# Kernel tuning notes

Hardware: AMD Instinct MI355X
Metric: run time of the kernel (lower is better)

Reference implementation:

```python
import jax, jax.numpy as jnp
import numpy as np

QMAX = 127.0  # 8-bit symmetric: levels in [-128, 127]


def _ste_round(v):
    # round with straight-through estimator (matches torch fake-quant training)
    return v + jax.lax.stop_gradient(jnp.round(v) - v)


def _act_fake_quant(x, clip_factor):
    # per-tensor symmetric fake quant with learnable clip (lac):
    # clip range = sigmoid(clip_factor) * max|x|
    scale = jax.nn.sigmoid(clip_factor) * jnp.max(jnp.abs(x)) / QMAX
    return jnp.clip(_ste_round(x / scale), -QMAX - 1.0, QMAX) * scale


def _weight_fake_quant(w):
    # per-output-channel symmetric fake quant; w: [out, in]
    scale = jnp.max(jnp.abs(w), axis=1, keepdims=True) / QMAX
    return jnp.clip(_ste_round(w / scale), -QMAX - 1.0, QMAX) * scale


def setup_inputs() -> dict:
    key = jax.random.key(0)
    k1, k2, k3, k4 = jax.random.split(key, 4)
    B, S, H, I = 8, 8192, 1024, 2816
    return {
        "x": jax.random.normal(k1, (B, S, H), dtype=jnp.float32),
        "clip_x": jnp.full((1,), 4.0, dtype=jnp.float32),     # sigmoid(4) ~ 0.982
        "clip_down": jnp.full((1,), 4.0, dtype=jnp.float32),
        "w_gate": jax.random.normal(k2, (I, H), dtype=jnp.float32) * 0.02,
        "w_up": jax.random.normal(k3, (I, H), dtype=jnp.float32) * 0.02,
        "w_down": jax.random.normal(k4, (H, I), dtype=jnp.float32) * 0.02,
    }


def reference(x, clip_x, clip_down, w_gate, w_up, w_down):
    # _trans_forward: quantize act -> gate/up quant-matmul -> SwiGLU -> quantize -> down quant-matmul
    xq = _act_fake_quant(x, clip_x[0])                       # [B,S,H]
    gate = jnp.einsum("bsh,ih->bsi", xq, _weight_fake_quant(w_gate))
    up = jnp.einsum("bsh,ih->bsi", xq, _weight_fake_quant(w_up))
    h = _act_fake_quant(jax.nn.silu(gate) * up, clip_down[0])  # [B,S,I]
    return jnp.einsum("bsi,hi->bsh", h, _weight_fake_quant(w_down))
```

## Files before the change

kernel.cpp:

```cpp
#include <hip/hip_runtime.h>
#include <stdint.h>

typedef __attribute__((ext_vector_type(4))) int i32x4;

typedef const __attribute__((address_space(1))) void gvoid_t;
typedef __attribute__((address_space(3))) void lvoid_t;

#define GLD16(g, l) __builtin_amdgcn_global_load_lds((gvoid_t*)(g), (lvoid_t*)(l), 16, 0, 0)
#define FENCE() asm volatile("" ::: "memory")
#define BARRIER() do { FENCE(); __builtin_amdgcn_s_barrier(); FENCE(); } while (0)
#define GATE4() asm volatile("s_waitcnt vmcnt(4)\n\ts_barrier" ::: "memory")
#define GATE0() asm volatile("s_waitcnt vmcnt(0)\n\ts_barrier" ::: "memory")

__device__ inline int q1mul(float x, float r) {
    return (int)fminf(fmaxf(rintf(x * r), -128.f), 127.f);
}
__device__ inline int q1div(float x, float s) {
    return (int)fminf(fmaxf(rintf(x / s), -128.f), 127.f);
}
__device__ inline int pack4(float4 v, float r) {
    return (q1mul(v.x, r) & 255) | ((q1mul(v.y, r) & 255) << 8) |
           ((q1mul(v.z, r) & 255) << 16) | ((q1mul(v.w, r) & 255) << 24);
}

__global__ void k_absmax(const float* __restrict__ x, size_t n4, unsigned int* __restrict__ out) {
    size_t S = (size_t)gridDim.x * blockDim.x;
    size_t i = (size_t)blockIdx.x * blockDim.x + threadIdx.x;
    const float4* x4 = (const float4*)x;
    float m0 = 0.f, m1 = 0.f, m2 = 0.f, m3 = 0.f;
    for (; i + 3 * S < n4; i += 4 * S) {
        float4 v0 = x4[i], v1 = x4[i + S], v2 = x4[i + 2 * S], v3 = x4[i + 3 * S];
        m0 = fmaxf(m0, fmaxf(fmaxf(fabsf(v0.x), fabsf(v0.y)), fmaxf(fabsf(v0.z), fabsf(v0.w))));
        m1 = fmaxf(m1, fmaxf(fmaxf(fabsf(v1.x), fabsf(v1.y)), fmaxf(fabsf(v1.z), fabsf(v1.w))));
        m2 = fmaxf(m2, fmaxf(fmaxf(fabsf(v2.x), fabsf(v2.y)), fmaxf(fabsf(v2.z), fabsf(v2.w))));
        m3 = fmaxf(m3, fmaxf(fmaxf(fabsf(v3.x), fabsf(v3.y)), fmaxf(fabsf(v3.z), fabsf(v3.w))));
    }
    for (; i < n4; i += S) {
        float4 v = x4[i];
        m0 = fmaxf(m0, fmaxf(fmaxf(fabsf(v.x), fabsf(v.y)), fmaxf(fabsf(v.z), fabsf(v.w))));
    }
    float m = fmaxf(fmaxf(m0, m1), fmaxf(m2, m3));
    #pragma unroll
    for (int off = 32; off > 0; off >>= 1) m = fmaxf(m, __shfl_xor(m, off, 64));
    if ((threadIdx.x & 63) == 0) atomicMax(out, __float_as_uint(m));
}

__global__ void k_scale(const float* __restrict__ clip, const unsigned int* __restrict__ maxbits,
                        float* __restrict__ s_out) {
    float m = __uint_as_float(*maxbits);
    float sig = 1.f / (1.f + expf(-clip[0]));
    float s = sig * m / 127.f;
    s_out[0] = s;
    s_out[1] = 1.f / s;
}

__global__ void k_quant_f32_i8(const float* __restrict__ in, int4* __restrict__ out,
                               const float* __restrict__ sptr, size_t n16) {
    float r = sptr[1];
    size_t S = (size_t)gridDim.x * blockDim.x;
    size_t i = (size_t)blockIdx.x * blockDim.x + threadIdx.x;
    const float4* in4 = (const float4*)in;
    for (; i < n16; i += S) {
        float4 v0 = in4[4 * i], v1 = in4[4 * i + 1], v2 = in4[4 * i + 2], v3 = in4[4 * i + 3];
        int4 o;
        o.x = pack4(v0, r); o.y = pack4(v1, r); o.z = pack4(v2, r); o.w = pack4(v3, r);
        out[i] = o;
    }
}

__global__ void k_quant_h16_i8(const short* __restrict__ h16, const float* __restrict__ sblk,
                               const float* __restrict__ sh, int4* __restrict__ qh, size_t nchunks) {
    const float rh = sh[1] * (1.f / 32766.f);
    size_t S = (size_t)gridDim.x * blockDim.x;
    size_t i = (size_t)blockIdx.x * blockDim.x + threadIdx.x;
    for (; i < nchunks; i += S) {
        int row = (int)(i / 176);
        int col = (int)(i - (size_t)row * 176) * 16;
        float f = sblk[(row >> 8) * 22 + (col >> 7)] * rh;
        const int4* p = (const int4*)(h16 + (size_t)row * 2816 + col);
        int4 lo = p[0], hi = p[1];
        int w[8] = {lo.x, lo.y, lo.z, lo.w, hi.x, hi.y, hi.z, hi.w};
        int ob[4];
        #pragma unroll
        for (int j = 0; j < 4; ++j) {
            int q0 = q1mul((float)(short)(w[2 * j] & 0xFFFF), f);
            int q1 = q1mul((float)(short)(w[2 * j] >> 16), f);
            int q2 = q1mul((float)(short)(w[2 * j + 1] & 0xFFFF), f);
            int q3 = q1mul((float)(short)(w[2 * j + 1] >> 16), f);
            ob[j] = (q0 & 255) | ((q1 & 255) << 8) | ((q2 & 255) << 16) | ((q3 & 255) << 24);
        }
        int4 o; o.x = ob[0]; o.y = ob[1]; o.z = ob[2]; o.w = ob[3];
        qh[i] = o;
    }
}

__global__ void k_quant_w_i8(const float* __restrict__ W, int8_t* __restrict__ Q,
                             float* __restrict__ srow, int cols) {
    int row = blockIdx.x;
    const float* w = W + (size_t)row * cols;
    float m = 0.f;
    for (int c = threadIdx.x; c < cols; c += 256) m = fmaxf(m, fabsf(w[c]));
    #pragma unroll
    for (int off = 32; off > 0; off >>= 1) m = fmaxf(m, __shfl_xor(m, off, 64));
    __shared__ float red[4];
    if ((threadIdx.x & 63) == 0) red[threadIdx.x >> 6] = m;
    __syncthreads();
    if (threadIdx.x == 0) {
        float mm = fmaxf(fmaxf(red[0], red[1]), fmaxf(red[2], red[3]));
        red[0] = mm / 127.f;
        srow[row] = mm / 127.f;
    }
    __syncthreads();
    float s = red[0];
    for (int c = threadIdx.x; c < cols; c += 256)
        Q[(size_t)row * cols + c] = (int8_t)q1div(w[c], s);
}

__global__ __launch_bounds__(512, 2) void k_gemm1_i8(
    const int8_t* __restrict__ Aq, const int8_t* __restrict__ Bg, const int8_t* __restrict__ Bu,
    const float* __restrict__ sg, const float* __restrict__ su, const float* __restrict__ sx,
    short* __restrict__ H16, float* __restrict__ sblk, unsigned int* __restrict__ maxh,
    int nt_base)
{
    constexpr int K = 1024, N = 2816, NT = K / 64, TB = 32768;
    __shared__ int8_t lds[131072];

    const int wgl = (int)blockIdx.x >> 3;
    const int xcd = (int)blockIdx.x & 7;
    const int mtspan = (int)(gridDim.x >> 3) / 11;
    const int mt = xcd * mtspan + wgl / 11;
    const int nt = nt_base + wgl % 11;
    const int m0 = mt * 256, n0 = nt * 128;
    const int tid = threadIdx.x;
    const int wid = tid >> 6, lane = tid & 63;
    const int wm = wid >> 2, wn = wid & 3;
    const int lr = lane & 15, lk = lane >> 4;

    const int srow = tid >> 2;
    const int scol = ((tid & 3) ^ ((srow >> 1) & 3)) << 4;
    const int8_t* gA0 = Aq + (size_t)(m0 + srow) * K + scol;
    const int8_t* gA1 = gA0 + (size_t)128 * K;
    const int8_t* gG  = Bg + (size_t)(n0 + srow) * K + scol;
    const int8_t* gU  = Bu + (size_t)(n0 + srow) * K + scol;
    const int ldst = wid << 10;

    const int swz = (lk ^ ((lr >> 1) & 3)) << 4;
    int offA[8], offG[2], offU[2];
    #pragma unroll
    for (int mi = 0; mi < 8; ++mi) offA[mi] = (wm * 128 + mi * 16 + lr) * 64 + swz;
    #pragma unroll
    for (int ni = 0; ni < 2; ++ni) {
        offG[ni] = 16384 + (wn * 32 + ni * 16 + lr) * 64 + swz;
        offU[ni] = 24576 + (wn * 32 + ni * 16 + lr) * 64 + swz;
    }

    i32x4 accg[8][2] = {};
    i32x4 accu[8][2] = {};

    auto stage1 = [&](int t, int q) {
        int8_t* L = &lds[(t % 3) * TB];
        const size_t k0 = (size_t)t * 64;
        if (q == 0)      GLD16(gA0 + k0, L + ldst);
        else if (q == 1) GLD16(gA1 + k0, L + 8192  + ldst);
        else if (q == 2) GLD16(gG  + k0, L + 16384 + ldst);
        else             GLD16(gU  + k0, L + 24576 + ldst);
    };

    #pragma unroll
    for (int q = 0; q < 4; ++q) stage1(0, q);
    #pragma unroll
    for (int q = 0; q < 4; ++q) stage1(1, q);
    GATE4();

    for (int t = 0; t < NT; ++t) {
        const int8_t* L = &lds[(t % 3) * TB];
        const bool st2 = (t + 2 < NT);
        i32x4 bg[2], bu[2];
        #pragma unroll
        for (int q = 0; q < 4; ++q) {
            i32x4 a0 = *(const i32x4*)(L + offA[2 * q]);
            i32x4 a1 = *(const i32x4*)(L + offA[2 * q + 1]);
            if (q == 0) {
                #pragma unroll
                for (int ni = 0; ni < 2; ++ni) {
                    bg[ni] = *(const i32x4*)(L + offG[ni]);
                    bu[ni] = *(const i32x4*)(L + offU[ni]);
                }
            }
            if (st2) stage1(t + 2, q);
            BARRIER();
            __builtin_amdgcn_s_setprio(1);
            #pragma unroll
            for (int ni = 0; ni < 2; ++ni) {
                accg[2 * q][ni]     = __builtin_amdgcn_mfma_i32_16x16x64_i8(a0, bg[ni], accg[2 * q][ni], 0, 0, 0);
                accu[2 * q][ni]     = __builtin_amdgcn_mfma_i32_16x16x64_i8(a0, bu[ni], accu[2 * q][ni], 0, 0, 0);
                accg[2 * q + 1][ni] = __builtin_amdgcn_mfma_i32_16x16x64_i8(a1, bg[ni], accg[2 * q + 1][ni], 0, 0, 0);
                accu[2 * q + 1][ni] = __builtin_amdgcn_mfma_i32_16x16x64_i8(a1, bu[ni], accu[2 * q + 1][ni], 0, 0, 0);
            }
            __builtin_amdgcn_s_setprio(0);
            if (q == 3) { if (st2) { GATE4(); } else { GATE0(); } }
            else        { BARRIER(); }
        }
    }

    const float s_x = sx[0];
    float lmax = 0.f;
    #pragma unroll
    for (int ni = 0; ni < 2; ++ni) {
        const int nl = wn * 32 + ni * 16 + lr;
        const float fg = s_x * sg[n0 + nl];
        const float fu = s_x * su[n0 + nl];
        #pragma unroll
        for (int mi = 0; mi < 8; ++mi) {
            const int rowb = wm * 128 + mi * 16 + lk * 4;
            #pragma unroll
            for (int r = 0; r < 4; ++r) {
                float g = (float)accg[mi][ni][r] * fg;
                float u = (float)accu[mi][ni][r] * fu;
                float h = g * u / (1.f + expf(-g));
                *(float*)(lds + ((rowb + r) << 9) + (nl << 2)) = h;
                lmax = fmaxf(lmax, fabsf(h));
            }
        }
    }
    #pragma unroll
    for (int off = 32; off > 0; off >>= 1) lmax = fmaxf(lmax, __shfl_xor(lmax, off, 64));
    unsigned int* slot = (unsigned int*)&sblk[mt * 22 + nt];
    if (lane == 0) atomicMax(slot, __float_as_uint(lmax));
    BARRIER();
    const float bmax = __uint_as_float(*slot);
    if (tid == 0) atomicMax(maxh, __float_as_uint(bmax));
    const float qs = 32766.f / fmaxf(bmax, 1e-20f);
    uint* H16u = (uint*)H16;
    #pragma unroll
    for (int k = 0; k < 32; ++k) {
        const int fidx = 2 * (tid + k * 512);
        const int row = fidx >> 7, c2 = fidx & 127;
        const float2 hv = *(const float2*)(lds + (fidx << 2));
        const int s0 = (int)rintf(hv.x * qs), s1 = (int)rintf(hv.y * qs);
        H16u[((size_t)(m0 + row) * N + n0 + c2) >> 1] = (s0 & 0xFFFF) | (s1 << 16);
    }
}

__global__ __launch_bounds__(512, 2) void k_gemm2_i8(
    const int8_t* __restrict__ Aq, const int8_t* __restrict__ Bw,
    const float* __restrict__ sw, const float* __restrict__ sh,
    float* __restrict__ Out)
{
    constexpr int K = 2816, N = 1024, NT = K / 64, TB = 32768;
    __shared__ int8_t lds[3 * TB];

    const int chunk = gridDim.x >> 3;
    const int wg = ((int)blockIdx.x & 7) * chunk + ((int)blockIdx.x >> 3);
    const int mt = wg >> 2, nt = wg & 3;
    const int m0 = mt * 256, n0 = nt * 256;
    const int tid = threadIdx.x;
    const int wid = tid >> 6, lane = tid & 63;
    const int wm = wid >> 2, wn = wid & 3;
    const int lr = lane & 15, lk = lane >> 4;

    const int srow = tid >> 2;
    const int scol = ((tid & 3) ^ ((srow >> 1) & 3)) << 4;
    const int8_t* gA0 = Aq + (size_t)(m0 + srow) * K + scol;
    const int8_t* gA1 = gA0 + (size_t)128 * K;
    const int8_t* gB0 = Bw + (size_t)(n0 + srow) * K + scol;
    const int8_t* gB1 = gB0 + (size_t)128 * K;
    const int ldst = wid << 10;

    const int swz = (lk ^ ((lr >> 1) & 3)) << 4;
    int offA[8], offB[4];
    #pragma unroll
    for (int mi = 0; mi < 8; ++mi) offA[mi] = (wm * 128 + mi * 16 + lr) * 64 + swz;
    #pragma unroll
    for (int ni = 0; ni < 4; ++ni) offB[ni] = 16384 + (wn * 64 + ni * 16 + lr) * 64 + swz;

    i32x4 acc[8][4] = {};

    auto stage1 = [&](int t, int q) {
        int8_t* L = &lds[(t % 3) * TB];
        const size_t k0 = (size_t)t * 64;
        if (q == 0)      GLD16(gA0 + k0, L + ldst);
        else if (q == 1) GLD16(gA1 + k0, L + 8192  + ldst);
        else if (q == 2) GLD16(gB0 + k0, L + 16384 + ldst);
        else             GLD16(gB1 + k0, L + 24576 + ldst);
    };

    #pragma unroll
    for (int q = 0; q < 4; ++q) stage1(0, q);
    #pragma unroll
    for (int q = 0; q < 4; ++q) stage1(1, q);
    GATE4();

    for (int t = 0; t < NT; ++t) {
        const int8_t* L = &lds[(t % 3) * TB];
        const bool st2 = (t + 2 < NT);
        i32x4 b[4];
        #pragma unroll
        for (int q = 0; q < 4; ++q) {
            i32x4 a0 = *(const i32x4*)(L + offA[2 * q]);
            i32x4 a1 = *(const i32x4*)(L + offA[2 * q + 1]);
            if (q == 0) {
                #pragma unroll
                for (int ni = 0; ni < 4; ++ni) b[ni] = *(const i32x4*)(L + offB[ni]);
            }
            if (st2) stage1(t + 2, q);
            BARRIER();
            __builtin_amdgcn_s_setprio(1);
            #pragma unroll
            for (int ni = 0; ni < 4; ++ni) {
                acc[2 * q][ni]     = __builtin_amdgcn_mfma_i32_16x16x64_i8(a0, b[ni], acc[2 * q][ni], 0, 0, 0);
                acc[2 * q + 1][ni] = __builtin_amdgcn_mfma_i32_16x16x64_i8(a1, b[ni], acc[2 * q + 1][ni], 0, 0, 0);
            }
            __builtin_amdgcn_s_setprio(0);
            if (q == 3) { if (st2) { GATE4(); } else { GATE0(); } }
            else        { BARRIER(); }
        }
    }

    const float s_h = sh[0];
    #pragma unroll
    for (int ni = 0; ni < 4; ++ni) {
        const int n = n0 + wn * 64 + ni * 16 + lr;
        const float f = s_h * sw[n];
        #pragma unroll
        for (int mi = 0; mi < 8; ++mi) {
            const int mb = m0 + wm * 128 + mi * 16 + lk * 4;
            #pragma unroll
            for (int r = 0; r < 4; ++r)
                Out[(size_t)(mb + r) * N + n] = (float)acc[mi][ni][r] * f;
        }
    }
}

extern "C" void kernel_launch(void* const* d_in, const int* in_sizes, int n_in,
                              void* d_out, int out_size, void* d_ws, size_t ws_size,
                              hipStream_t stream) {
    const float* x       = (const float*)d_in[0];
    const float* clip_x  = (const float*)d_in[1];
    const float* clip_dn = (const float*)d_in[2];
    const float* w_gate  = (const float*)d_in[3];
    const float* w_up    = (const float*)d_in[4];
    const float* w_down  = (const float*)d_in[5];
    float* out = (float*)d_out;

    const int Hd = 1024, Id = 2816;
    const int M = in_sizes[0] / Hd;
    const size_t nx = (size_t)M * Hd;
    const size_t nh = (size_t)M * Id;

    char* ws = (char*)d_ws;
    size_t off = 0;
    auto alloc = [&](size_t bytes) -> char* {
        char* p = ws + off;
        off = (off + bytes + 255) & ~(size_t)255;
        return p;
    };
    unsigned int* max_slots = (unsigned int*)alloc(8);
    float* sxp = (float*)alloc(8);
    float* shp = (float*)alloc(8);
    int8_t* qx  = (int8_t*)alloc(nx);
    int8_t* qwg = (int8_t*)alloc((size_t)Id * Hd);
    int8_t* qwu = (int8_t*)alloc((size_t)Id * Hd);
    int8_t* qwd = (int8_t*)alloc((size_t)Hd * Id);
    float* swg = (float*)alloc((size_t)Id * 4);
    float* swu = (float*)alloc((size_t)Id * 4);
    float* swd = (float*)alloc((size_t)Hd * 4);
    int8_t* qh = (int8_t*)alloc(nh);
    short* h16 = (short*)alloc(nh * 2);
    const size_t sblk_bytes = (size_t)(M / 256) * 22 * 4;
    float* sblk = (float*)alloc(sblk_bytes);

    hipMemsetAsync(max_slots, 0, 8, stream);
    hipMemsetAsync(sblk, 0, sblk_bytes, stream);

    k_absmax<<<4096, 256, 0, stream>>>(x, nx / 4, &max_slots[0]);
    k_scale<<<1, 1, 0, stream>>>(clip_x, &max_slots[0], sxp);
    k_quant_f32_i8<<<2048, 256, 0, stream>>>(x, (int4*)qx, sxp, nx / 16);
    k_quant_w_i8<<<Id, 256, 0, stream>>>(w_gate, qwg, swg, Hd);
    k_quant_w_i8<<<Id, 256, 0, stream>>>(w_up, qwu, swu, Hd);
    k_quant_w_i8<<<Hd, 256, 0, stream>>>(w_down, qwd, swd, Id);

    const int g1grid = (M / 256) * 11;
    k_gemm1_i8<<<g1grid, 512, 0, stream>>>(qx, qwg, qwu, swg, swu, sxp, h16, sblk, &max_slots[1], 0);
    k_gemm1_i8<<<g1grid, 512, 0, stream>>>(qx, qwg, qwu, swg, swu, sxp, h16, sblk, &max_slots[1], 11);
    k_scale<<<1, 1, 0, stream>>>(clip_dn, &max_slots[1], shp);
    k_quant_h16_i8<<<4096, 256, 0, stream>>>(h16, sblk, shp, (int4*)qh, nh / 16);

    k_gemm2_i8<<<(M / 256) * (Hd / 256), 512, 0, stream>>>(qh, qwd, swd, shp, out);
}
```

Measured before the change: 1.151 ms.

## Deepen int8 GEMM pipeline to four LDS stages with inline-asm LDS reads

Both int8 GEMM kernels move from a 3-buffer to a 4-buffer LDS ring and prefetch three k-tiles ahead, with the vmcnt gates retuned to match. LDS fragment reads are now issued through inline ds_read_b128 with immediate offsets from one base address instead of per-fragment offset arrays, followed by explicit lgkmcnt waits and sched barriers. The aim is to hide more global-load latency and cut address arithmetic in the inner loop. The cost is 128KB of LDS per block, which may lower occupancy below the declared two blocks per CU. Hand-placed waits also restrict how the compiler can schedule instructions.

```diff
diff --git a/kernel.cpp b/kernel.cpp
--- a/kernel.cpp
+++ b/kernel.cpp
@@ -9,8 +9,16 @@
 #define GLD16(g, l) __builtin_amdgcn_global_load_lds((gvoid_t*)(g), (lvoid_t*)(l), 16, 0, 0)
 #define FENCE() asm volatile("" ::: "memory")
 #define BARRIER() do { FENCE(); __builtin_amdgcn_s_barrier(); FENCE(); } while (0)
+#define SBAR() asm volatile("s_barrier" ::: "memory")
+#define LGKM0() do { asm volatile("s_waitcnt lgkmcnt(0)" ::: "memory"); __builtin_amdgcn_sched_barrier(0); } while (0)
+#define GATE8() asm volatile("s_waitcnt vmcnt(8)\n\ts_barrier" ::: "memory")
 #define GATE4() asm volatile("s_waitcnt vmcnt(4)\n\ts_barrier" ::: "memory")
 #define GATE0() asm volatile("s_waitcnt vmcnt(0)\n\ts_barrier" ::: "memory")
+
+#define DSR2(d0, d1, addr, O0, O1)                                  \
+    asm volatile("ds_read_b128 %0, %2 offset:" O0 "\n\t"            \
+                 "ds_read_b128 %1, %2 offset:" O1                   \
+                 : "=v"(d0), "=v"(d1) : "v"(addr))
 
 __device__ inline int q1mul(float x, float r) {
     return (int)fminf(fmaxf(rintf(x * r), -128.f), 127.f);
@@ -145,20 +153,16 @@
     const int ldst = wid << 10;
 
     const int swz = (lk ^ ((lr >> 1) & 3)) << 4;
-    int offA[8], offG[2], offU[2];
-    #pragma unroll
-    for (int mi = 0; mi < 8; ++mi) offA[mi] = (wm * 128 + mi * 16 + lr) * 64 + swz;
-    #pragma unroll
-    for (int ni = 0; ni < 2; ++ni) {
-        offG[ni] = 16384 + (wn * 32 + ni * 16 + lr) * 64 + swz;
-        offU[ni] = 24576 + (wn * 32 + ni * 16 + lr) * 64 + swz;
-    }
+    const unsigned ldsBase = (unsigned)(size_t)&lds[0];
+    const unsigned aoff = (unsigned)((wm * 128 + lr) * 64 + swz);
+    const unsigned boff = (unsigned)(16384 + (wn * 32 + lr) * 64 + swz);
 
     i32x4 accg[8][2] = {};
     i32x4 accu[8][2] = {};
+    i32x4 bg[2], bu[2];
 
     auto stage1 = [&](int t, int q) {
-        int8_t* L = &lds[(t % 3) * TB];
+        int8_t* L = &lds[(t & 3) * TB];
         const size_t k0 = (size_t)t * 64;
         if (q == 0)      GLD16(gA0 + k0, L + ldst);
         else if (q == 1) GLD16(gA1 + k0, L + 8192  + ldst);
@@ -170,38 +174,57 @@
     for (int q = 0; q < 4; ++q) stage1(0, q);
     #pragma unroll
     for (int q = 0; q < 4; ++q) stage1(1, q);
-    GATE4();
+    #pragma unroll
+    for (int q = 0; q < 4; ++q) stage1(2, q);
+    GATE8();
+
+#define G1_MFMA(Q, A0, A1)                                                                     \
+    __builtin_amdgcn_s_setprio(1);                                                             \
+    _Pragma("unroll")                                                                          \
+    for (int ni = 0; ni < 2; ++ni) {                                                           \
+        accg[2 * (Q)][ni]     = __builtin_amdgcn_mfma_i32_16x16x64_i8(A0, bg[ni], accg[2 * (Q)][ni], 0, 0, 0);     \
+        accu[2 * (Q)][ni]     = __builtin_amdgcn_mfma_i32_16x16x64_i8(A0, bu[ni], accu[2 * (Q)][ni], 0, 0, 0);     \
+        accg[2 * (Q) + 1][ni] = __builtin_amdgcn_mfma_i32_16x16x64_i8(A1, bg[ni], accg[2 * (Q) + 1][ni], 0, 0, 0); \
+        accu[2 * (Q) + 1][ni] = __builtin_amdgcn_mfma_i32_16x16x64_i8(A1, bu[ni], accu[2 * (Q) + 1][ni], 0, 0, 0); \
+    }                                                                                          \
+    __builtin_amdgcn_s_setprio(0);
 
     for (int t = 0; t < NT; ++t) {
-        const int8_t* L = &lds[(t % 3) * TB];
-        const bool st2 = (t + 2 < NT);
-        i32x4 bg[2], bu[2];
-        #pragma unroll
-        for (int q = 0; q < 4; ++q) {
-            i32x4 a0 = *(const i32x4*)(L + offA[2 * q]);
-            i32x4 a1 = *(const i32x4*)(L + offA[2 * q + 1]);
-            if (q == 0) {
-                #pragma unroll
-                for (int ni = 0; ni < 2; ++ni) {
-                    bg[ni] = *(const i32x4*)(L + offG[ni]);
-                    bu[ni] = *(const i32x4*)(L + offU[ni]);
-                }
-            }
-            if (st2) stage1(t + 2, q);
-            BARRIER();
-            __builtin_amdgcn_s_setprio(1);
-            #pragma unroll
-            for (int ni = 0; ni < 2; ++ni) {
-                accg[2 * q][ni]     = __builtin_amdgcn_mfma_i32_16x16x64_i8(a0, bg[ni], accg[2 * q][ni], 0, 0, 0);
-                accu[2 * q][ni]     = __builtin_amdgcn_mfma_i32_16x16x64_i8(a0, bu[ni], accu[2 * q][ni], 0, 0, 0);
-                accg[2 * q + 1][ni] = __builtin_amdgcn_mfma_i32_16x16x64_i8(a1, bg[ni], accg[2 * q + 1][ni], 0, 0, 0);
-                accu[2 * q + 1][ni] = __builtin_amdgcn_mfma_i32_16x16x64_i8(a1, bu[ni], accu[2 * q + 1][ni], 0, 0, 0);
-            }
-            __builtin_amdgcn_s_setprio(0);
-            if (q == 3) { if (st2) { GATE4(); } else { GATE0(); } }
-            else        { BARRIER(); }
-        }
-    }
+        const unsigned bufb = ldsBase + ((unsigned)(t & 3) << 15);
+        const unsigned aAddr = bufb + aoff, bAddr = bufb + boff;
+        const bool st3 = (t + 3 < NT);
+        i32x4 a0, a1;
+
+        DSR2(a0, a1, aAddr, "0", "1024");
+        DSR2(bg[0], bg[1], bAddr, "0", "1024");
+        DSR2(bu[0], bu[1], bAddr, "8192", "9216");
+        if (st3) stage1(t + 3, 0);
+        SBAR(); LGKM0();
+        G1_MFMA(0, a0, a1)
+        SBAR();
+
+        DSR2(a0, a1, aAddr, "2048", "3072");
+        if (st3) stage1(t + 3, 1);
+        SBAR(); LGKM0();
+        G1_MFMA(1, a0, a1)
+        SBAR();
+
+        DSR2(a0, a1, aAddr, "4096", "5120");
+        if (st3) stage1(t + 3, 2);
+        SBAR(); LGKM0();
+        G1_MFMA(2, a0, a1)
+        SBAR();
+
+        DSR2(a0, a1, aAddr, "6144", "7168");
+        if (st3) stage1(t + 3, 3);
+        SBAR(); LGKM0();
+        G1_MFMA(3, a0, a1)
+        if (t + 3 < NT)      { GATE8(); }
+        else if (t + 2 < NT) { GATE4(); }
+        else if (t + 1 < NT) { GATE0(); }
+        else                 { SBAR(); }
+    }
+#undef G1_MFMA
 
     const float s_x = sx[0];
     float lmax = 0.f;
@@ -248,7 +271,7 @@
     float* __restrict__ Out)
 {
     constexpr int K = 2816, N = 1024, NT = K / 64, TB = 32768;
-    __shared__ int8_t lds[3 * TB];
+    __shared__ int8_t lds[131072];
 
     const int chunk = gridDim.x >> 3;
     const int wg = ((int)blockIdx.x & 7) * chunk + ((int)blockIdx.x >> 3);
@@ -268,16 +291,15 @@
     const int ldst = wid << 10;
 
     const int swz = (lk ^ ((lr >> 1) & 3)) << 4;
-    int offA[8], offB[4];
-    #pragma unroll
-    for (int mi = 0; mi < 8; ++mi) offA[mi] = (wm * 128 + mi * 16 + lr) * 64 + swz;
-    #pragma unroll
-    for (int ni = 0; ni < 4; ++ni) offB[ni] = 16384 + (wn * 64 + ni * 16 + lr) * 64 + swz;
+    const unsigned ldsBase = (unsigned)(size_t)&lds[0];
+    const unsigned aoff = (unsigned)((wm * 128 + lr) * 64 + swz);
+    const unsigned boff = (unsigned)(16384 + (wn * 64 + lr) * 64 + swz);
 
     i32x4 acc[8][4] = {};
+    i32x4 b[4];
 
     auto stage1 = [&](int t, int q) {
-        int8_t* L = &lds[(t % 3) * TB];
+        int8_t* L = &lds[(t & 3) * TB];
         const size_t k0 = (size_t)t * 64;
         if (q == 0)      GLD16(gA0 + k0, L + ldst);
         else if (q == 1) GLD16(gA1 + k0, L + 8192  + ldst);
@@ -289,33 +311,55 @@
     for (int q = 0; q < 4; ++q) stage1(0, q);
     #pragma unroll
     for (int q = 0; q < 4; ++q) stage1(1, q);
-    GATE4();
+    #pragma unroll
+    for (int q = 0; q < 4; ++q) stage1(2, q);
+    GATE8();
+
+#define G2_MFMA(Q, A0, A1)                                                                     \
+    __builtin_amdgcn_s_setprio(1);                                                             \
+    _Pragma("unroll")                                                                          \
+    for (int ni = 0; ni < 4; ++ni) {                                                           \
+        acc[2 * (Q)][ni]     = __builtin_amdgcn_mfma_i32_16x16x64_i8(A0, b[ni], acc[2 * (Q)][ni], 0, 0, 0);     \
+        acc[2 * (Q) + 1][ni] = __builtin_amdgcn_mfma_i32_16x16x64_i8(A1, b[ni], acc[2 * (Q) + 1][ni], 0, 0, 0); \
+    }                                                                                          \
+    __builtin_amdgcn_s_setprio(0);
 
     for (int t = 0; t < NT; ++t) {
-        const int8_t* L = &lds[(t % 3) * TB];
-        const bool st2 = (t + 2 < NT);
-        i32x4 b[4];
-        #pragma unroll
-        for (int q = 0; q < 4; ++q) {
-            i32x4 a0 = *(const i32x4*)(L + offA[2 * q]);
-            i32x4 a1 = *(const i32x4*)(L + offA[2 * q + 1]);
-            if (q == 0) {
-                #pragma unroll
-                for (int ni = 0; ni < 4; ++ni) b[ni] = *(const i32x4*)(L + offB[ni]);
-            }
-            if (st2) stage1(t + 2, q);
-            BARRIER();
-            __builtin_amdgcn_s_setprio(1);
-            #pragma unroll
-            for (int ni = 0; ni < 4; ++ni) {
-                acc[2 * q][ni]     = __builtin_amdgcn_mfma_i32_16x16x64_i8(a0, b[ni], acc[2 * q][ni], 0, 0, 0);
-                acc[2 * q + 1][ni] = __builtin_amdgcn_mfma_i32_16x16x64_i8(a1, b[ni], acc[2 * q + 1][ni], 0, 0, 0);
-            }
-            __builtin_amdgcn_s_setprio(0);
-            if (q == 3) { if (st2) { GATE4(); } else { GATE0(); } }
-            else        { BARRIER(); }
-        }
-    }
+        const unsigned bufb = ldsBase + ((unsigned)(t & 3) << 15);
+        const unsigned aAddr = bufb + aoff, bAddr = bufb + boff;
+        const bool st3 = (t + 3 < NT);
+        i32x4 a0, a1;
+
+        DSR2(a0, a1, aAddr, "0", "1024");
+        DSR2(b[0], b[1], bAddr, "0", "1024");
+        DSR2(b[2], b[3], bAddr, "2048", "3072");
+        if (st3) stage1(t + 3, 0);
+        SBAR(); LGKM0();
+        G2_MFMA(0, a0, a1)
+        SBAR();
+
+        DSR2(a0, a1, aAddr, "2048", "3072");
+        if (st3) stage1(t + 3, 1);
+        SBAR(); LGKM0();
+        G2_MFMA(1, a0, a1)
+        SBAR();
+
+        DSR2(a0, a1, aAddr, "4096", "5120");
+        if (st3) stage1(t + 3, 2);
+        SBAR(); LGKM0();
+        G2_MFMA(2, a0, a1)
+        SBAR();
+
+        DSR2(a0, a1, aAddr, "6144", "7168");
+        if (st3) stage1(t + 3, 3);
+        SBAR(); LGKM0();
+        G2_MFMA(3, a0, a1)
+        if (t + 3 < NT)      { GATE8(); }
+        else if (t + 2 < NT) { GATE4(); }
+        else if (t + 1 < NT) { GATE0(); }
+        else                 { SBAR(); }
+    }
+#undef G2_MFMA
 
     const float s_h = sh[0];
     #pragma unroll
```

New measurement: 1.201 ms. +4.3%, slower.
